# Performance work log

Measured on AMD Instinct MI355X. Metric: run time of the kernel, lower is better.

## Reference

```python
import jax, jax.numpy as jnp
import numpy as np

GRID = 32
SCALE_FACTOR = 0.2
EPS = 1e-12


def _compute_phi(verts, faces, G):
    """Unsigned distance-to-mesh on a GxGxG grid over [-1,1]^3, zeroed outside the mesh.
    Returns phi[z, y, x] (grid_sample D,H,W layout). verts [V,3], faces [F,3] int.
    Matches the SDF CUDA kernel semantics: phi = penetration depth (dist inside, 0 outside)."""
    v0 = verts[faces[:, 0]]  # [F,3]
    v1 = verts[faces[:, 1]]
    v2 = verts[faces[:, 2]]
    e0 = v1 - v0             # [F,3]
    e1 = v2 - v0
    a = jnp.sum(e0 * e0, -1)             # [F]
    b = jnp.sum(e0 * e1, -1)
    c = jnp.sum(e1 * e1, -1)

    lin = jnp.linspace(-1.0, 1.0, G, dtype=verts.dtype)
    zz, yy, xx = jnp.meshgrid(lin, lin, lin, indexing='ij')
    pts = jnp.stack([xx, yy, zz], -1).reshape(-1, 3)   # [P,3], coords (x,y,z), P=G^3

    # --- point-to-triangle squared distance, all [P,F] after one [P,F,3] temp ---
    w = pts[:, None, :] - v0[None, :, :]               # [P,F,3]
    f = jnp.sum(w * w, -1)                             # |p-v0|^2   [P,F]
    de0 = jnp.sum(w * e0, -1)                          # (p-v0).e0  [P,F]
    de1 = jnp.sum(w * e1, -1)                          # (p-v0).e1  [P,F]

    det = a * c - b * b                                # [F]
    det_s = jnp.where(det > EPS, det, 1.0)
    u = (c * de0 - b * de1) / det_s                    # barycentric of plane projection
    v = (a * de1 - b * de0) / det_s
    inside_tri = (u >= 0) & (v >= 0) & (u + v <= 1) & (det > EPS)
    plane_d2 = f - (u * de0 + v * de1)                 # squared dist to plane point

    # edge v0->v1
    a_s = jnp.where(a > EPS, a, 1.0)
    t0 = jnp.clip(de0 / a_s, 0.0, 1.0)
    d2_0 = f - 2.0 * t0 * de0 + t0 * t0 * a
    # edge v0->v2
    c_s = jnp.where(c > EPS, c, 1.0)
    t1 = jnp.clip(de1 / c_s, 0.0, 1.0)
    d2_1 = f - 2.0 * t1 * de1 + t1 * t1 * c
    # edge v1->v2: e2 = e1-e0; w1 = p - v1 = w - e0
    ee2 = a + c - 2.0 * b                              # |e2|^2
    ee2_s = jnp.where(ee2 > EPS, ee2, 1.0)
    dot2 = de1 - de0 - (b - a)                         # w1.e2
    w1sq = f - 2.0 * de0 + a                           # |w1|^2
    t2 = jnp.clip(dot2 / ee2_s, 0.0, 1.0)
    d2_2 = w1sq - 2.0 * t2 * dot2 + t2 * t2 * ee2

    edge_d2 = jnp.minimum(jnp.minimum(d2_0, d2_1), d2_2)
    d2 = jnp.where(inside_tri, plane_d2, edge_d2)
    d2 = jnp.maximum(d2, 0.0)
    dist = jnp.sqrt(jnp.min(d2, axis=1))               # [P]

    # --- inside/outside via +z ray casting parity ---
    x0, y0, z0 = v0[:, 0], v0[:, 1], v0[:, 2]
    x1, y1, z1 = v1[:, 0], v1[:, 1], v1[:, 2]
    x2, y2, z2 = v2[:, 0], v2[:, 1], v2[:, 2]
    det2 = (x1 - x0) * (y2 - y0) - (x2 - x0) * (y1 - y0)   # [F]
    det2_s = jnp.where(jnp.abs(det2) > EPS, det2, 1.0)
    px = pts[:, 0:1]; py = pts[:, 1:2]; pz = pts[:, 2:3]   # [P,1]
    u2 = ((px - x0) * (y2 - y0) - (py - y0) * (x2 - x0)) / det2_s  # [P,F]
    v2b = ((x1 - x0) * (py - y0) - (y1 - y0) * (px - x0)) / det2_s
    in2d = (u2 >= 0) & (v2b >= 0) & (u2 + v2b <= 1) & (jnp.abs(det2) > EPS)
    zint = z0 + u2 * (z1 - z0) + v2b * (z2 - z0)
    hits = jnp.sum((in2d & (zint > pz)).astype(jnp.int32), axis=1)  # [P]
    inside_mesh = (hits % 2).astype(dist.dtype)

    phi = dist * inside_mesh                           # >= 0 everywhere
    return phi.reshape(G, G, G)                        # [z, y, x]


def _trilinear_zeros(phi, q):
    """torch grid_sample(mode=bilinear, padding=zeros, align_corners=True) on a
    [G,G,G] (z,y,x) volume at points q [N,3] with coords (x,y,z) in [-1,1]."""
    G = phi.shape[0]
    fidx = (q + 1.0) * 0.5 * (G - 1)                   # [N,3] float indices (x,y,z)
    i0 = jnp.floor(fidx).astype(jnp.int32)
    w1 = fidx - i0.astype(fidx.dtype)
    w0 = 1.0 - w1
    out = jnp.zeros(q.shape[0], dtype=phi.dtype)
    for dz in (0, 1):
        for dy in (0, 1):
            for dx in (0, 1):
                ix = i0[:, 0] + dx
                iy = i0[:, 1] + dy
                iz = i0[:, 2] + dz
                valid = (ix >= 0) & (ix < G) & (iy >= 0) & (iy < G) & (iz >= 0) & (iz < G)
                val = phi[jnp.clip(iz, 0, G - 1), jnp.clip(iy, 0, G - 1), jnp.clip(ix, 0, G - 1)]
                wgt = ((w1[:, 0] if dx else w0[:, 0]) *
                       (w1[:, 1] if dy else w0[:, 1]) *
                       (w1[:, 2] if dz else w0[:, 2]))
                out = out + jnp.where(valid, val * wgt, 0.0)
    return out


def _sdf_loss(human_verts, object_verts, faces):
    sg = jax.lax.stop_gradient
    # bounding boxes (computed under no_grad in the original)
    bmin_h = jnp.min(human_verts, axis=0); bmax_h = jnp.max(human_verts, axis=0)
    bmin_o = jnp.min(object_verts, axis=0); bmax_o = jnp.max(object_verts, axis=0)
    overlap = jnp.all(bmin_h <= bmax_o) & jnp.all(bmin_o <= bmax_h)

    center = sg(0.5 * (bmin_h + bmax_h))                               # [3]
    scale = sg((1.0 + SCALE_FACTOR) * 0.5 * jnp.max(bmax_h - bmin_h))  # scalar

    hv_scaled = sg((human_verts - center) / scale)      # in [-1,1]^3 by construction
    phi = sg(_compute_phi(hv_scaled, faces, GRID))      # [G,G,G], no_grad in original

    q = (object_verts - center) / scale                 # grads flow to object_verts
    phi_val = _trilinear_zeros(phi, q)                  # [N]
    loss = jnp.sum(phi_val) ** 2
    return jnp.where(overlap, loss, jnp.zeros((), dtype=loss.dtype))


def setup_inputs() -> dict:
    key = jax.random.key(0)
    k1, k2, k3 = jax.random.split(key, 3)
    human_verts = jax.random.normal(k1, (778, 3), dtype=jnp.float32)
    object_verts = jax.random.normal(k2, (4096, 3), dtype=jnp.float32)
    faces = jax.random.randint(k3, (1538, 3), 0, 778, dtype=jnp.int32)
    return {"human_verts": human_verts, "object_verts": object_verts, "faces": faces}


def reference(human_verts, object_verts, faces):
    return _sdf_loss(human_verts, object_verts, faces)
```

## Files before the change

kernel.cpp:

```cpp
#include <hip/hip_runtime.h>

#define EPSF 1e-12f
#define GN 32
#define NPTS (GN * GN * GN)
#define NCOL (GN * GN)
#define FSPLIT 16
#define NCG 16
#define NBLK (NCG * FSPLIT)
#define NTHR 1024
#define NWAVES (NBLK * (NTHR / 64))
#define MAXCH 160
#define CAP 10240

__device__ __forceinline__ float dot_rn(const float* x, const float* y) {
    return __fadd_rn(__fadd_rn(__fmul_rn(x[0], y[0]), __fmul_rn(x[1], y[1])),
                     __fmul_rn(x[2], y[2]));
}
__device__ __forceinline__ float wmin64(float v) {
    for (int o = 32; o > 0; o >>= 1) v = fminf(v, __shfl_xor(v, o));
    return v;
}
__device__ __forceinline__ float wmax64(float v) {
    for (int o = 32; o > 0; o >>= 1) v = fmaxf(v, __shfl_xor(v, o));
    return v;
}
__device__ __forceinline__ float wsum64(float v) {
    for (int o = 32; o > 0; o >>= 1) v += __shfl_xor(v, o);
    return v;
}
__device__ __forceinline__ float gridc(int g) {
    return __fadd_rn(-1.0f, __fmul_rn((float)g, 2.0f / 31.0f));
}

__device__ __forceinline__ void frec(const float* __restrict__ hv,
                                     const int* __restrict__ faces, int f,
                                     float cx, float cy, float cz, float sc,
                                     float* o) {
    const float qnan = __int_as_float(0x7FC00000);
    int ia = faces[3 * f + 0], ib = faces[3 * f + 1], ic = faces[3 * f + 2];
    float v0[3], v1[3], v2[3];
    for (int k = 0; k < 3; ++k) {
        float cen = (k == 0) ? cx : ((k == 1) ? cy : cz);
        v0[k] = __fdiv_rn(__fsub_rn(hv[3 * ia + k], cen), sc);
        v1[k] = __fdiv_rn(__fsub_rn(hv[3 * ib + k], cen), sc);
        v2[k] = __fdiv_rn(__fsub_rn(hv[3 * ic + k], cen), sc);
    }
    float e0[3], e1[3];
    for (int k = 0; k < 3; ++k) {
        e0[k] = __fsub_rn(v1[k], v0[k]);
        e1[k] = __fsub_rn(v2[k], v0[k]);
    }
    float a = dot_rn(e0, e0);
    float b = dot_rn(e0, e1);
    float cc = dot_rn(e1, e1);
    float det = __fsub_rn(__fmul_rn(a, cc), __fmul_rn(b, b));
    float inv_det = (det > EPSF) ? (1.0f / det) : qnan;
    float inv_a = 1.0f / ((a > EPSF) ? a : 1.0f);
    float inv_c = 1.0f / ((cc > EPSF) ? cc : 1.0f);
    float ee2 = __fsub_rn(__fadd_rn(a, cc), __fmul_rn(2.0f, b));
    float inv_ee2 = 1.0f / ((ee2 > EPSF) ? ee2 : 1.0f);
    float det2 = __fsub_rn(__fmul_rn(e0[0], e1[1]), __fmul_rn(e1[0], e0[1]));
    float inv_det2s = (fabsf(det2) > EPSF) ? (1.0f / det2) : qnan;
    o[0] = v0[0]; o[1] = v0[1]; o[2] = v0[2];
    o[3] = e0[0]; o[4] = e0[1]; o[5] = e0[2];
    o[6] = e1[0]; o[7] = e1[1]; o[8] = e1[2];
    o[9] = a; o[10] = b; o[11] = cc;
    o[12] = inv_det; o[13] = inv_a; o[14] = inv_c;
    o[15] = ee2; o[16] = inv_ee2; o[17] = inv_det2s;
    o[18] = __fsub_rn(b, a); o[19] = 0.f;
}

__device__ __forceinline__ float celld2(const float* r, float px, float py, float pz) {
    float wx = __fsub_rn(px, r[0]), wy = __fsub_rn(py, r[1]), wz = __fsub_rn(pz, r[2]);
    float ff = wx * wx + wy * wy + wz * wz;
    float de0 = wx * r[3] + wy * r[4] + wz * r[5];
    float de1 = wx * r[6] + wy * r[7] + wz * r[8];
    float u = (r[11] * de0 - r[10] * de1) * r[12];
    float v = (r[9] * de1 - r[10] * de0) * r[12];
    bool inside = (u >= 0.0f) & (v >= 0.0f) & (u + v <= 1.0f);
    float plane_d2 = ff - (u * de0 + v * de1);
    float t0 = fminf(fmaxf(de0 * r[13], 0.0f), 1.0f);
    float d2_0 = ff + t0 * (t0 * r[9] - 2.0f * de0);
    float t1 = fminf(fmaxf(de1 * r[14], 0.0f), 1.0f);
    float d2_1 = ff + t1 * (t1 * r[11] - 2.0f * de1);
    float dot2 = (de1 - de0) - r[18];
    float w1sq = ff - 2.0f * de0 + r[9];
    float t2 = fminf(fmaxf(dot2 * r[16], 0.0f), 1.0f);
    float d2_2 = w1sq + t2 * (t2 * r[15] - 2.0f * dot2);
    float ed2 = fminf(fminf(d2_0, d2_1), d2_2);
    float d2 = inside ? plane_d2 : ed2;
    return fmaxf(d2, 0.0f);
}

__global__ void __launch_bounds__(NTHR) k_all(
    const float* __restrict__ hv, int nh,
    const float* __restrict__ ov, int no,
    const int* __restrict__ faces, int nf,
    unsigned* __restrict__ d2u, unsigned* __restrict__ parm,
    unsigned* __restrict__ counter, float* __restrict__ out)
{
    __shared__ float s_fd[MAXCH * 20];
    __shared__ unsigned s_sm[NPTS / 32];
    __shared__ unsigned s_clist[CAP];
    __shared__ unsigned s_cnt[16];
    __shared__ unsigned s_pm[64];
    __shared__ float s_w[16][12];
    __shared__ float s_hdr[4];
    __shared__ float s_hb[6];
    __shared__ unsigned s_last;

    int t = threadIdx.x, lane = t & 63, wvid = t >> 6;
    int fs = blockIdx.x >> 4;
    int cg = blockIdx.x & 15;
    const float step = 2.0f / 31.0f;

    for (int i = t; i < NPTS / 32; i += NTHR) s_sm[i] = 0u;
    if (t < 64) s_pm[t] = 0u;

    {
        float mnx = INFINITY, mny = INFINITY, mnz = INFINITY;
        float mxx = -INFINITY, mxy = -INFINITY, mxz = -INFINITY;
        for (int i = t; i < nh; i += NTHR) {
            float x = hv[3 * i], y = hv[3 * i + 1], z = hv[3 * i + 2];
            mnx = fminf(mnx, x); mny = fminf(mny, y); mnz = fminf(mnz, z);
            mxx = fmaxf(mxx, x); mxy = fmaxf(mxy, y); mxz = fmaxf(mxz, z);
        }
        mnx = wmin64(mnx); mny = wmin64(mny); mnz = wmin64(mnz);
        mxx = wmax64(mxx); mxy = wmax64(mxy); mxz = wmax64(mxz);
        if (lane == 0) {
            s_w[wvid][0] = mnx; s_w[wvid][1] = mny; s_w[wvid][2] = mnz;
            s_w[wvid][3] = mxx; s_w[wvid][4] = mxy; s_w[wvid][5] = mxz;
        }
        __syncthreads();
        if (wvid == 0) {
            float a0 = (lane < 16) ? s_w[lane][0] : INFINITY;
            float a1 = (lane < 16) ? s_w[lane][1] : INFINITY;
            float a2 = (lane < 16) ? s_w[lane][2] : INFINITY;
            float a3 = (lane < 16) ? s_w[lane][3] : -INFINITY;
            float a4 = (lane < 16) ? s_w[lane][4] : -INFINITY;
            float a5 = (lane < 16) ? s_w[lane][5] : -INFINITY;
            a0 = wmin64(a0); a1 = wmin64(a1); a2 = wmin64(a2);
            a3 = wmax64(a3); a4 = wmax64(a4); a5 = wmax64(a5);
            if (lane == 0) {
                float e0 = __fsub_rn(a3, a0);
                float e1 = __fsub_rn(a4, a1);
                float e2 = __fsub_rn(a5, a2);
                float m = fmaxf(e0, fmaxf(e1, e2));
                s_hdr[0] = __fmul_rn(0.5f, __fadd_rn(a0, a3));
                s_hdr[1] = __fmul_rn(0.5f, __fadd_rn(a1, a4));
                s_hdr[2] = __fmul_rn(0.5f, __fadd_rn(a2, a5));
                s_hdr[3] = __fmul_rn(0.6f, m);
                s_hb[0] = a0; s_hb[1] = a1; s_hb[2] = a2;
                s_hb[3] = a3; s_hb[4] = a4; s_hb[5] = a5;
            }
        }
        __syncthreads();
    }
    float cx = s_hdr[0], cy = s_hdr[1], cz = s_hdr[2], sc = s_hdr[3];

    int chunkB = (nf + FSPLIT - 1) / FSPLIT;
    int f0B = fs * chunkB;
    int nloc = min(nf, f0B + chunkB) - f0B;
    for (int i = t; i < nloc; i += NTHR)
        frec(hv, faces, f0B + i, cx, cy, cz, sc, s_fd + i * 20);
    for (int j = t; j < no; j += NTHR) {
        float qx = __fdiv_rn(__fsub_rn(ov[3 * j + 0], cx), sc);
        float qy = __fdiv_rn(__fsub_rn(ov[3 * j + 1], cy), sc);
        float qz = __fdiv_rn(__fsub_rn(ov[3 * j + 2], cz), sc);
        float fx = __fmul_rn(__fmul_rn(__fadd_rn(qx, 1.0f), 0.5f), 31.0f);
        float fy = __fmul_rn(__fmul_rn(__fadd_rn(qy, 1.0f), 0.5f), 31.0f);
        float fz = __fmul_rn(__fmul_rn(__fadd_rn(qz, 1.0f), 0.5f), 31.0f);
        int ix0 = (int)floorf(fx), iy0 = (int)floorf(fy), iz0 = (int)floorf(fz);
        for (int dz = 0; dz < 2; ++dz)
            for (int dy = 0; dy < 2; ++dy)
                for (int dx = 0; dx < 2; ++dx) {
                    int ix = ix0 + dx, iy = iy0 + dy, iz = iz0 + dz;
                    if ((ix >= 0) & (ix < GN) & (iy >= 0) & (iy < GN) &
                        (iz >= 0) & (iz < GN)) {
                        unsigned cell = (unsigned)((iz * GN + iy) * GN + ix);
                        atomicOr(&s_sm[cell >> 5], 1u << (cell & 31u));
                    }
                }
    }
    __syncthreads();

    {
        int col = cg * 64 + lane;
        int gx = col & 31, gy = col >> 5;
        float px = __fadd_rn(-1.0f, __fmul_rn((float)gx, step));
        float py = __fadd_rn(-1.0f, __fmul_rn((float)gy, step));
        int i0 = __builtin_amdgcn_readfirstlane((wvid * nloc) / 16);
        int i1 = __builtin_amdgcn_readfirstlane(((wvid + 1) * nloc) / 16);

        unsigned cmask = 0u;
        for (int i = i0; i < i1; ++i) {
            const float* q = s_fd + i * 20;
            float v0x = q[0], v0y = q[1], v0z = q[2];
            float e0x = q[3], e0y = q[4], e0z = q[5];
            float e1x = q[6], e1y = q[7], e1z = q[8];
            float inv_det2s = q[17];

            float wx = __fsub_rn(px, v0x), wy = __fsub_rn(py, v0y);
            float u2n = __fsub_rn(__fmul_rn(wx, e1y), __fmul_rn(wy, e1x));
            float v2n = __fsub_rn(__fmul_rn(e0x, wy), __fmul_rn(e0y, wx));
            float u2 = __fmul_rn(u2n, inv_det2s);
            float v2 = __fmul_rn(v2n, inv_det2s);
            bool in2d = (u2 >= 0.0f) & (v2 >= 0.0f) & (__fadd_rn(u2, v2) <= 1.0f);
            float zint = __fadd_rn(__fadd_rn(v0z, __fmul_rn(u2, e0z)), __fmul_rn(v2, e1z));
            int c = 0;
            {
                float p;
                p = __fadd_rn(-1.0f, __fmul_rn((float)(15), step));      if (zint > p) c = 16;
                p = __fadd_rn(-1.0f, __fmul_rn((float)(c + 7), step));   if (zint > p) c += 8;
                p = __fadd_rn(-1.0f, __fmul_rn((float)(c + 3), step));   if (zint > p) c += 4;
                p = __fadd_rn(-1.0f, __fmul_rn((float)(c + 1), step));   if (zint > p) c += 2;
                p = __fadd_rn(-1.0f, __fmul_rn((float)(c), step));       if (zint > p) c += 1;
                p = __fadd_rn(-1.0f, __fmul_rn((float)(c), step));       if (zint > p) c += 1;
            }
            unsigned mask = (c == 0) ? 0u : (0xffffffffu >> (32 - c));
            cmask ^= in2d ? mask : 0u;
        }
        atomicXor(&s_pm[lane], cmask);
        __syncthreads();
        if (t < 64) atomicXor(&parm[cg * 64 + t], s_pm[t]);
    }

    unsigned nc;
    {
        unsigned cnt = 0;
        for (int chunk = wvid * 32; chunk < wvid * 32 + 32; ++chunk) {
            unsigned cid = (unsigned)(chunk * 64 + lane);
            bool present = (s_sm[cid >> 5] >> (cid & 31u)) & 1u;
            cnt += (unsigned)__popcll(__ballot(present));
        }
        if (lane == 0) s_cnt[wvid] = cnt;
        __syncthreads();
        unsigned base = 0;
        for (int wv = 0; wv < wvid; ++wv) base += s_cnt[wv];
        nc = base;
        for (int wv = wvid; wv < 16; ++wv) nc += s_cnt[wv];
        if (nc <= CAP) {
            for (int chunk = wvid * 32; chunk < wvid * 32 + 32; ++chunk) {
                unsigned cid = (unsigned)(chunk * 64 + lane);
                bool present = (s_sm[cid >> 5] >> (cid & 31u)) & 1u;
                unsigned long long bal = __ballot(present);
                unsigned pre = (unsigned)__popcll(bal & ((1ull << lane) - 1ull));
                if (present) s_clist[base + pre] = cid;
                base += (unsigned)__popcll(bal);
            }
        }
        __syncthreads();
    }

    {
        bool uselist = nc <= CAP;
        unsigned nbatch = uselist ? ((nc + 15) >> 4) : (NPTS / 16);
        int nfb = (nf + 63) >> 6;
        unsigned ntiles = nbatch * (unsigned)nfb;
        unsigned w = (unsigned)(blockIdx.x * 16 + wvid);

        for (unsigned tt = w; tt < ntiles; tt += NWAVES) {
            unsigned cb = tt / (unsigned)nfb;
            unsigned fb = tt - cb * (unsigned)nfb;
            int f = (int)(fb * 64u) + lane;
            if (f >= nf) f = 0;
            float r[20];
            frec(hv, faces, f, cx, cy, cz, sc, r);

            float myres = 0.0f; unsigned mycid = 0u; bool mine = false;
            for (int j = 0; j < 16; ++j) {
                unsigned idx = cb * 16u + (unsigned)j;
                unsigned cid; bool cvalid;
                if (uselist) {
                    cvalid = idx < nc;
                    cid = cvalid ? s_clist[idx] : 0u;
                } else {
                    cid = idx;
                    cvalid = (idx < (unsigned)NPTS) &&
                             ((s_sm[cid >> 5] >> (cid & 31u)) & 1u);
                }
                if (!cvalid) continue;
                int gx = (int)(cid & 31u), gy = (int)((cid >> 5) & 31u),
                    gz = (int)(cid >> 10);
                float m = celld2(r, gridc(gx), gridc(gy), gridc(gz));
                for (int o = 32; o > 0; o >>= 1) m = fminf(m, __shfl_xor(m, o));
                if (lane == j) { myres = m; mycid = cid; mine = true; }
            }
            if (mine) atomicMin(&d2u[mycid], __float_as_uint(myres));
        }
    }

    __syncthreads();
    if (t == 0) {
        unsigned old = atomicAdd(counter, 1u);
        s_last = (old == (unsigned)(NBLK - 2)) ? 1u : 0u;
    }
    __syncthreads();
    if (s_last == 0u) return;

    {
        float onx = INFINITY, ony = INFINITY, onz = INFINITY;
        float oxx = -INFINITY, oxy = -INFINITY, oxz = -INFINITY;
        for (int j = t; j < no; j += NTHR) {
            float x = ov[3 * j], y = ov[3 * j + 1], z = ov[3 * j + 2];
            onx = fminf(onx, x); ony = fminf(ony, y); onz = fminf(onz, z);
            oxx = fmaxf(oxx, x); oxy = fmaxf(oxy, y); oxz = fmaxf(oxz, z);
        }
        onx = wmin64(onx); ony = wmin64(ony); onz = wmin64(onz);
        oxx = wmax64(oxx); oxy = wmax64(oxy); oxz = wmax64(oxz);
        if (lane == 0) {
            s_w[wvid][0] = onx; s_w[wvid][1] = ony; s_w[wvid][2] = onz;
            s_w[wvid][3] = oxx; s_w[wvid][4] = oxy; s_w[wvid][5] = oxz;
        }
        __syncthreads();
        if (t == 0) {
            float a0 = INFINITY, a1 = INFINITY, a2 = INFINITY;
            float a3 = -INFINITY, a4 = -INFINITY, a5 = -INFINITY;
            for (int wv = 0; wv < 16; ++wv) {
                a0 = fminf(a0, s_w[wv][0]); a1 = fminf(a1, s_w[wv][1]);
                a2 = fminf(a2, s_w[wv][2]); a3 = fmaxf(a3, s_w[wv][3]);
                a4 = fmaxf(a4, s_w[wv][4]); a5 = fmaxf(a5, s_w[wv][5]);
            }
            bool ovl = (s_hb[0] <= a3) && (s_hb[1] <= a4) && (s_hb[2] <= a5) &&
                       (a0 <= s_hb[3]) && (a1 <= s_hb[4]) && (a2 <= s_hb[5]);
            s_hdr[0] = ovl ? 1.0f : 0.0f;
        }
        __syncthreads();
        float ovl = s_hdr[0];
        float acc = 0.0f;
        for (int j = t; j < no; j += NTHR) {
            float qx = __fdiv_rn(__fsub_rn(ov[3 * j + 0], cx), sc);
            float qy = __fdiv_rn(__fsub_rn(ov[3 * j + 1], cy), sc);
            float qz = __fdiv_rn(__fsub_rn(ov[3 * j + 2], cz), sc);
            float fx = __fmul_rn(__fmul_rn(__fadd_rn(qx, 1.0f), 0.5f), 31.0f);
            float fy = __fmul_rn(__fmul_rn(__fadd_rn(qy, 1.0f), 0.5f), 31.0f);
            float fz = __fmul_rn(__fmul_rn(__fadd_rn(qz, 1.0f), 0.5f), 31.0f);
            float flx = floorf(fx), fly = floorf(fy), flz = floorf(fz);
            int ix0 = (int)flx, iy0 = (int)fly, iz0 = (int)flz;
            float w1x = __fsub_rn(fx, flx), w0x = __fsub_rn(1.0f, w1x);
            float w1y = __fsub_rn(fy, fly), w0y = __fsub_rn(1.0f, w1y);
            float w1z = __fsub_rn(fz, flz), w0z = __fsub_rn(1.0f, w1z);
            for (int dy = 0; dy < 2; ++dy)
                for (int dx = 0; dx < 2; ++dx) {
                    int ix = ix0 + dx, iy = iy0 + dy;
                    bool okxy = (ix >= 0) & (ix < GN) & (iy >= 0) & (iy < GN);
                    unsigned pm = 0u;
                    if (okxy) {
                        unsigned pmv = __hip_atomic_load(&parm[iy * GN + ix],
                                         __ATOMIC_RELAXED, __HIP_MEMORY_SCOPE_AGENT);
                        pm = pmv ^ 0xFFFFFFFFu;
                    }
                    for (int dz = 0; dz < 2; ++dz) {
                        int iz = iz0 + dz;
                        bool ok = okxy & (iz >= 0) & (iz < GN);
                        if (ok && ((pm >> iz) & 1u)) {
                            unsigned du = __hip_atomic_load(
                                &d2u[(iz * GN + iy) * GN + ix],
                                __ATOMIC_RELAXED, __HIP_MEMORY_SCOPE_AGENT);
                            float val = sqrtf(__uint_as_float(du));
                            float wgt = __fmul_rn(
                                __fmul_rn(dx ? w1x : w0x, dy ? w1y : w0y),
                                dz ? w1z : w0z);
                            acc = __fadd_rn(acc, __fmul_rn(val, wgt));
                        }
                    }
                }
        }
        acc = wsum64(acc);
        if (lane == 0) s_w[wvid][6] = acc;
        __syncthreads();
        if (wvid == 0) {
            float v = (lane < 16) ? s_w[lane][6] : 0.0f;
            v = wsum64(v);
            if (lane == 0) {
                float loss = __fmul_rn(v, v);
                out[0] = (ovl != 0.0f) ? loss : 0.0f;
            }
        }
    }
}

extern "C" void kernel_launch(void* const* d_in, const int* in_sizes, int n_in,
                              void* d_out, int out_size, void* d_ws, size_t ws_size,
                              hipStream_t stream) {
    const float* hv = (const float*)d_in[0];
    const float* ov = (const float*)d_in[1];
    const int* faces = (const int*)d_in[2];
    int nh = in_sizes[0] / 3;
    int no = in_sizes[1] / 3;
    int nf = in_sizes[2] / 3;

    unsigned* d2u = (unsigned*)d_ws;
    unsigned* parm = d2u + NPTS;
    unsigned* counter = parm + NCOL;

    hipMemsetAsync(d_ws, 0xFF, (size_t)(NPTS + NCOL + 16) * 4, stream);
    k_all<<<NBLK, NTHR, 0, stream>>>(hv, nh, ov, no, faces, nf,
                                     d2u, parm, counter, (float*)d_out);
}
```

Before: 126.5 us.

## Reorganize cell-face loop: lanes own cells, waves split cached faces, LDS min-reduce

```diff
diff --git a/kernel.cpp b/kernel.cpp
--- a/kernel.cpp
+++ b/kernel.cpp
@@ -8,9 +8,8 @@
 #define NCG 16
 #define NBLK (NCG * FSPLIT)
 #define NTHR 1024
-#define NWAVES (NBLK * (NTHR / 64))
 #define MAXCH 160
-#define CAP 10240
+#define CAP 8192
 
 __device__ __forceinline__ float dot_rn(const float* x, const float* y) {
     return __fadd_rn(__fadd_rn(__fmul_rn(x[0], y[0]), __fmul_rn(x[1], y[1])),
@@ -104,6 +103,7 @@
     __shared__ unsigned s_clist[CAP];
     __shared__ unsigned s_cnt[16];
     __shared__ unsigned s_pm[64];
+    __shared__ unsigned s_dm[64];
     __shared__ float s_w[16][12];
     __shared__ float s_hdr[4];
     __shared__ float s_hb[6];
@@ -254,39 +254,33 @@
 
     {
         bool uselist = nc <= CAP;
-        unsigned nbatch = uselist ? ((nc + 15) >> 4) : (NPTS / 16);
-        int nfb = (nf + 63) >> 6;
-        unsigned ntiles = nbatch * (unsigned)nfb;
-        unsigned w = (unsigned)(blockIdx.x * 16 + wvid);
-
-        for (unsigned tt = w; tt < ntiles; tt += NWAVES) {
-            unsigned cb = tt / (unsigned)nfb;
-            unsigned fb = tt - cb * (unsigned)nfb;
-            int f = (int)(fb * 64u) + lane;
-            if (f >= nf) f = 0;
-            float r[20];
-            frec(hv, faces, f, cx, cy, cz, sc, r);
-
-            float myres = 0.0f; unsigned mycid = 0u; bool mine = false;
-            for (int j = 0; j < 16; ++j) {
-                unsigned idx = cb * 16u + (unsigned)j;
-                unsigned cid; bool cvalid;
-                if (uselist) {
-                    cvalid = idx < nc;
-                    cid = cvalid ? s_clist[idx] : 0u;
-                } else {
-                    cid = idx;
-                    cvalid = (idx < (unsigned)NPTS) &&
-                             ((s_sm[cid >> 5] >> (cid & 31u)) & 1u);
-                }
-                if (!cvalid) continue;
-                int gx = (int)(cid & 31u), gy = (int)((cid >> 5) & 31u),
-                    gz = (int)(cid >> 10);
-                float m = celld2(r, gridc(gx), gridc(gy), gridc(gz));
-                for (int o = 32; o > 0; o >>= 1) m = fminf(m, __shfl_xor(m, o));
-                if (lane == j) { myres = m; mycid = cid; mine = true; }
-            }
-            if (mine) atomicMin(&d2u[mycid], __float_as_uint(myres));
+        unsigned nbatch = uselist ? ((nc + 63) >> 6) : (NPTS / 64);
+        int i0 = __builtin_amdgcn_readfirstlane((wvid * nloc) / 16);
+        int i1 = __builtin_amdgcn_readfirstlane(((wvid + 1) * nloc) / 16);
+
+        for (unsigned cb = (unsigned)cg; cb < nbatch; cb += 16) {
+            if (t < 64) s_dm[t] = 0x7f800000u;
+            __syncthreads();
+            unsigned idx = cb * 64 + (unsigned)lane;
+            bool cvalid; unsigned cid;
+            if (uselist) { cvalid = idx < nc; cid = cvalid ? s_clist[idx] : 0u; }
+            else { cid = idx; cvalid = (s_sm[cid >> 5] >> (cid & 31u)) & 1u; }
+            int gx = (int)(cid & 31u), gy = (int)((cid >> 5) & 31u),
+                gz = (int)(cid >> 10);
+            float px = gridc(gx), py = gridc(gy), pz = gridc(gz);
+            float dmin = 3.402823466e38f;
+            for (int i = i0; i < i1; ++i)
+                dmin = fminf(dmin, celld2(s_fd + i * 20, px, py, pz));
+            if (cvalid) atomicMin(&s_dm[lane], __float_as_uint(dmin));
+            __syncthreads();
+            if (t < 64) {
+                unsigned idx2 = cb * 64 + (unsigned)t;
+                bool v2; unsigned c2;
+                if (uselist) { v2 = idx2 < nc; c2 = v2 ? s_clist[idx2] : 0u; }
+                else { c2 = idx2; v2 = (s_sm[c2 >> 5] >> (c2 & 31u)) & 1u; }
+                if (v2) atomicMin(&d2u[c2], s_dm[t]);
+            }
+            __syncthreads();
         }
     }
 
```

Result: faster. 109.5 us (-13.5%).
